# Kernel tuning notes

Measured on AMD Instinct MI355X. Metric: run time of the kernel, lower is better.

The kernel has to match this reference:

```python
import jax, jax.numpy as jnp
import numpy as np

N, S, R, M, C, CZ = 1, 128, 256, 256, 32, 128


def setup_inputs() -> dict:
    key = jax.random.key(0)
    k1, k2, k3, k4 = jax.random.split(key, 4)
    return {
        "msa_repr": jax.random.normal(k1, (N, S, R, M), dtype=jnp.float32) * 0.1,
        "left_w": jax.random.normal(k2, (M, C), dtype=jnp.float32) * 0.02,
        "right_w": jax.random.normal(k3, (M, C), dtype=jnp.float32) * 0.02,
        "out_w": jax.random.normal(k4, (C * C, CZ), dtype=jnp.float32) * 0.02,
    }


def reference(msa_repr, left_w, right_w, out_w):
    # msa_repr: [N,S,R,M]
    n, s, r, m = msa_repr.shape
    c = left_w.shape[1]
    # opm_projection: [N,S,R,M] @ [M,C] -> [N,S,R,C]
    left = jnp.einsum('nsrm,mc->nsrc', msa_repr, left_w)
    right = jnp.einsum('nsrm,mc->nsrc', msa_repr, right_w)
    # outer product summed over MSA dim s: [N,R,T,C,C]
    # (torch: a=left.transpose(-2,-3) -> [N,R,S,C]; einsum '...bac,...dae->...bdce')
    outer = jnp.einsum('nsrc,nste->nrtce', left, right).reshape(n, r, r, c * c)
    # project to pair channel: [N,R,T,C*C] @ [C*C,CZ] -> [N,R,T,CZ]
    return jnp.matmul(outer, out_w)
```

## Files before the change

### kernel.cpp

```cpp
#include <hip/hip_runtime.h>
#include <stdint.h>

#define S_DIM 128
#define R_DIM 256
#define M_DIM 256
#define C_DIM 32
#define CZ_DIM 128
#define K2_DIM 1024

typedef _Float16 f16;
typedef _Float16 f16x4 __attribute__((ext_vector_type(4)));
typedef _Float16 f16x8 __attribute__((ext_vector_type(8)));
typedef float f32x4 __attribute__((ext_vector_type(4)));
typedef float f32x16 __attribute__((ext_vector_type(16)));

typedef const __attribute__((address_space(1))) uint32_t gu32_t;
typedef __attribute__((address_space(3))) uint32_t lu32_t;
#define GLOAD_LDS16(g, l) \
    __builtin_amdgcn_global_load_lds((gu32_t*)(g), (lu32_t*)(l), 16, 0, 0)

__global__ __launch_bounds__(256, 4)
void proj_kernel(const float* __restrict__ msa, const float* __restrict__ lw,
                 const float* __restrict__ rw, const float* __restrict__ ow,
                 f16* __restrict__ left_t, f16* __restrict__ rt2,
                 f16* __restrict__ wt2) {
    __shared__ __align__(16) f16 wlT[8192];
    __shared__ __align__(16) f16 wrT[8192];

    int bid = blockIdx.x;
    int tid = threadIdx.x;
    int w = tid >> 6;
    int lane = tid & 63;
    int q = lane >> 4, li = lane & 15;
    int r  = bid >> 1;
    int s0 = (bid & 1) << 6;
    int s_col = s0 + w * 16 + li;

    const f32x4* bp = (const f32x4*)(msa + ((size_t)s_col * R_DIM + r) * M_DIM + q * 8);
    f32x4 b[16];
#pragma unroll
    for (int ks = 0; ks < 8; ks++) { b[2 * ks] = bp[ks * 8]; b[2 * ks + 1] = bp[ks * 8 + 1]; }

    {
        int i = bid * 256 + tid;
        int cz = i >> 10, k2 = i & 1023;
        int c = k2 >> 5, e = k2 & 31;
        int k2p = ((e >> 2) << 7) + (c << 2) + (e & 3);
        int ntile = cz >> 5, l31o = cz & 31;
        int kk = k2p >> 4, q5o = (k2p >> 3) & 1, j = k2p & 7;
        wt2[(ntile * 64 + kk) * 512 + (l31o * 2 + q5o) * 8 + j] = (f16)ow[k2 * CZ_DIM + cz];
    }
#pragma unroll
    for (int k = 0; k < 32; k++) {
        int i = k * 256 + tid;
        int m = i >> 5, c = i & 31;
        int d = ((m >> 3) * 32 + c) * 8 + (m & 7);
        wlT[d] = (f16)lw[i];
        wrT[d] = (f16)rw[i];
    }
    __syncthreads();

    f32x4 aL0 = {0,0,0,0}, aL1 = {0,0,0,0}, aR0 = {0,0,0,0}, aR1 = {0,0,0,0};
#pragma unroll
    for (int ks = 0; ks < 8; ks++) {
        f16x8 bf;
#pragma unroll
        for (int u = 0; u < 4; u++) { bf[u] = (f16)b[2*ks][u]; bf[4 + u] = (f16)b[2*ks+1][u]; }
        const f16* a0 = wlT + ((ks * 4 + q) * 32 + li) * 8;
        const f16* a1 = wrT + ((ks * 4 + q) * 32 + li) * 8;
        f16x8 al0 = *(const f16x8*)(a0);
        f16x8 al1 = *(const f16x8*)(a0 + 128);
        f16x8 ar0 = *(const f16x8*)(a1);
        f16x8 ar1 = *(const f16x8*)(a1 + 128);
        aL0 = __builtin_amdgcn_mfma_f32_16x16x32_f16(al0, bf, aL0, 0, 0, 0);
        aL1 = __builtin_amdgcn_mfma_f32_16x16x32_f16(al1, bf, aL1, 0, 0, 0);
        aR0 = __builtin_amdgcn_mfma_f32_16x16x32_f16(ar0, bf, aR0, 0, 0, 0);
        aR1 = __builtin_amdgcn_mfma_f32_16x16x32_f16(ar1, bf, aR1, 0, 0, 0);
    }
    int ks_s = s_col >> 4, q5_s = (s_col >> 3) & 1, j_s = s_col & 7;
    int sbase = (r * 8 + ks_s) * 512 + q5_s * 8 + j_s;
    int rl = r & 7;
    f16* Lb = left_t + (size_t)(r >> 3) * 32768;
    int sc = s_col >> 3, sj = s_col & 7;
#pragma unroll
    for (int reg = 0; reg < 4; reg++) {
        int c0 = q * 4 + reg;
        int row0 = rl * 32 + c0;
        int swz = sc ^ c0;
        Lb[(row0 * 16 + swz) * 8 + sj]        = (f16)aL0[reg];
        Lb[((row0 + 16) * 16 + swz) * 8 + sj] = (f16)aL1[reg];
        rt2[sbase + c0 * 16]        = (f16)aR0[reg];
        rt2[sbase + (c0 + 16) * 16] = (f16)aR1[reg];
    }
}

__global__ __launch_bounds__(512, 4)
void fuse_kernel(const f16* __restrict__ left_t, const f16* __restrict__ rt2,
                 const f16* __restrict__ wt2, float* __restrict__ out) {
    __shared__ __align__(16) char lds[65536];
    f16* Ls = (f16*)lds;

    int bid = blockIdx.x;
    int br = bid >> 6, bt = bid & 63;
    int tid = threadIdx.x;
    int w = tid >> 6, lane = tid & 63;
    int q5 = lane >> 5, l31 = lane & 31, lx = lane & 15;

    const f16* Lg = left_t + (size_t)br * 32768;

#pragma unroll
    for (int it = 0; it < 8; it++) {
        GLOAD_LDS16(Lg + (size_t)(it * 512 + tid) * 8, Ls + (it * 512 + tid) * 8);
    }

    int t_tile = w & 3, rg4 = w >> 2;
    int g = bt * 4 + t_tile;
    const f16* ap = rt2 + (size_t)g * 4096 + (l31 * 2 + q5) * 8;
    f16x8 afr[8];
#pragma unroll
    for (int ks = 0; ks < 8; ks++) afr[ks] = *(const f16x8*)(ap + ks * 512);

    __syncthreads();

    f32x16 acc[4] = {};
#pragma unroll
    for (int i = 0; i < 4; i++) {
        const f16* bbase = Ls + ((rg4 * 4 + i) * 32 + l31) * 128;
#pragma unroll
        for (int ks = 0; ks < 8; ks++) {
            f16x8 bfr = *(const f16x8*)(bbase + (((2 * ks + q5) ^ lx) << 3));
            acc[i] = __builtin_amdgcn_mfma_f32_32x32x16_f16(afr[ks], bfr, acc[i], 0, 0, 0);
        }
    }

    int ntile = w & 3, kh = w >> 2;
    const f16* wbase = wt2 + (size_t)(ntile * 64 + kh * 32) * 512 + (l31 * 2 + q5) * 8;
    f16x8 wfg[8][4];
#pragma unroll
    for (int u = 0; u < 4; u++) wfg[0][u] = *(const f16x8*)(wbase + u * 512);

    __syncthreads();

    int chc = l31 >> 1, bsub = 8 * (l31 & 1);
#pragma unroll
    for (int i = 0; i < 4; i++) {
        int p = (rg4 * 4 + i) * 4 + t_tile;
        char* prow = lds + p * 2048;
#pragma unroll
        for (int rg = 0; rg < 4; rg++) {
            int ch = (2 * rg + q5) * 16 + chc;
            int phys = (ch + p) & 127;
            f16x4 h = {(f16)acc[i][4 * rg], (f16)acc[i][4 * rg + 1],
                       (f16)acc[i][4 * rg + 2], (f16)acc[i][4 * rg + 3]};
            *(f16x4*)(prow + phys * 16 + bsub) = h;
        }
    }
    __syncthreads();

    const char* lbase = lds + l31 * 2048;
    int base = 64 * kh + q5 + l31;
    f16x8 afg[8][4];
    f32x16 accA = {}, accB = {};
#pragma unroll
    for (int gg = 0; gg < 8; gg++) {
        if (gg == 0) {
#pragma unroll
            for (int u = 0; u < 4; u++) wfg[1][u] = *(const f16x8*)(wbase + (4 + u) * 512);
#pragma unroll
            for (int u = 0; u < 4; u++) wfg[2][u] = *(const f16x8*)(wbase + (8 + u) * 512);
#pragma unroll
            for (int u = 0; u < 4; u++)
                afg[0][u] = *(const f16x8*)(lbase + (((base + 2 * u) & 127) << 4));
#pragma unroll
            for (int u = 0; u < 4; u++)
                afg[1][u] = *(const f16x8*)(lbase + (((base + 8 + 2 * u) & 127) << 4));
        } else {
            if (gg + 2 < 8) {
#pragma unroll
                for (int u = 0; u < 4; u++)
                    wfg[gg + 2][u] = *(const f16x8*)(wbase + ((gg + 2) * 4 + u) * 512);
            }
            if (gg + 1 < 8) {
#pragma unroll
                for (int u = 0; u < 4; u++)
                    afg[gg + 1][u] = *(const f16x8*)(lbase + (((base + (gg + 1) * 8 + 2 * u) & 127) << 4));
            }
        }
        accA = __builtin_amdgcn_mfma_f32_32x32x16_f16(afg[gg][0], wfg[gg][0], accA, 0, 0, 0);
        accB = __builtin_amdgcn_mfma_f32_32x32x16_f16(afg[gg][1], wfg[gg][1], accB, 0, 0, 0);
        accA = __builtin_amdgcn_mfma_f32_32x32x16_f16(afg[gg][2], wfg[gg][2], accA, 0, 0, 0);
        accB = __builtin_amdgcn_mfma_f32_32x32x16_f16(afg[gg][3], wfg[gg][3], accB, 0, 0, 0);
    }
    f32x16 acc2;
#pragma unroll
    for (int v = 0; v < 16; v++) acc2[v] = accA[v] + accB[v];
    __syncthreads();

    if (w >= 4) {
        char* rb = lds + (w - 4) * 4096 + lane * 64;
#pragma unroll
        for (int u = 0; u < 4; u++) {
            f32x4 part = {acc2[4 * u], acc2[4 * u + 1], acc2[4 * u + 2], acc2[4 * u + 3]};
            *(f32x4*)(rb + u * 16) = part;
        }
    }
    __syncthreads();
    if (w < 4) {
        const char* rb = lds + w * 4096 + lane * 64;
#pragma unroll
        for (int u = 0; u < 4; u++) {
            f32x4 part = *(const f32x4*)(rb + u * 16);
#pragma unroll
            for (int v = 0; v < 4; v++) acc2[4 * u + v] += part[v];
        }
        int r0 = br * 8, t0 = bt * 4, cz = w * 32 + l31;
#pragma unroll
        for (int reg = 0; reg < 16; reg++) {
            int p = (reg & 3) + 8 * (reg >> 2) + 4 * q5;
            out[((size_t)((r0 + (p >> 2)) * R_DIM + t0 + (p & 3))) * CZ_DIM + cz] = acc2[reg];
        }
    }
}

extern "C" void kernel_launch(void* const* d_in, const int* in_sizes, int n_in,
                              void* d_out, int out_size, void* d_ws, size_t ws_size,
                              hipStream_t stream) {
    const float* msa = (const float*)d_in[0];
    const float* lw  = (const float*)d_in[1];
    const float* rw  = (const float*)d_in[2];
    const float* ow  = (const float*)d_in[3];
    char* ws = (char*)d_ws;
    f16* left_t = (f16*)(ws);
    f16* rt2    = (f16*)(ws + (size_t)2 * 1024 * 1024);
    f16* wt2    = (f16*)(ws + (size_t)4 * 1024 * 1024);
    float* out  = (float*)d_out;

    proj_kernel<<<dim3(512), dim3(256), 0, stream>>>(msa, lw, rw, ow, left_t, rt2, wt2);
    fuse_kernel<<<dim3(2048), dim3(512), 0, stream>>>(left_t, rt2, wt2, out);
}
```

Baseline: 131.7 us.

## Process four row blocks per fuse workgroup with prefetched left tiles

Each fuse workgroup now loops over four consecutive row blocks. The right-side fragments and the first weight fragments are loaded once and reused across them. The next left tile is streamed into a separate LDS region while the current projection GEMM runs, using 128KB of dynamic shared memory and a launch bound of 2 waves per EU. This cuts redundant global loads and per-block setup, but it quarters the grid size and lowers occupancy, which may leave compute units underused.

```diff
diff --git a/kernel.cpp b/kernel.cpp
--- a/kernel.cpp
+++ b/kernel.cpp
@@ -94,130 +94,146 @@
     }
 }
 
-__global__ __launch_bounds__(512, 4)
+__global__ __launch_bounds__(512, 2)
 void fuse_kernel(const f16* __restrict__ left_t, const f16* __restrict__ rt2,
                  const f16* __restrict__ wt2, float* __restrict__ out) {
-    __shared__ __align__(16) char lds[65536];
+    extern __shared__ __align__(16) char lds[];
     f16* Ls = (f16*)lds;
+    char* Pr = lds + 65536;
 
     int bid = blockIdx.x;
-    int br = bid >> 6, bt = bid & 63;
+    int brq = bid >> 6, bt = bid & 63;
     int tid = threadIdx.x;
     int w = tid >> 6, lane = tid & 63;
     int q5 = lane >> 5, l31 = lane & 31, lx = lane & 15;
 
-    const f16* Lg = left_t + (size_t)br * 32768;
-
-#pragma unroll
-    for (int it = 0; it < 8; it++) {
-        GLOAD_LDS16(Lg + (size_t)(it * 512 + tid) * 8, Ls + (it * 512 + tid) * 8);
-    }
-
     int t_tile = w & 3, rg4 = w >> 2;
+    int ntile = w & 3, kh = w >> 2;
+
+    {
+        const f16* Lg = left_t + (size_t)(brq * 4) * 32768;
+#pragma unroll
+        for (int it = 0; it < 8; it++)
+            GLOAD_LDS16(Lg + (size_t)(it * 512 + tid) * 8, Ls + (it * 512 + tid) * 8);
+    }
+
     int g = bt * 4 + t_tile;
     const f16* ap = rt2 + (size_t)g * 4096 + (l31 * 2 + q5) * 8;
     f16x8 afr[8];
 #pragma unroll
     for (int ks = 0; ks < 8; ks++) afr[ks] = *(const f16x8*)(ap + ks * 512);
 
+    const f16* wbase = wt2 + (size_t)(ntile * 64 + kh * 32) * 512 + (l31 * 2 + q5) * 8;
+    const char* lbase = Pr + l31 * 2048;
+    int base = 64 * kh + q5 + l31;
+
+    f16x8 wfg[8][4];
+#pragma unroll
+    for (int u = 0; u < 4; u++) wfg[0][u] = *(const f16x8*)(wbase + u * 512);
+
     __syncthreads();
 
-    f32x16 acc[4] = {};
-#pragma unroll
-    for (int i = 0; i < 4; i++) {
-        const f16* bbase = Ls + ((rg4 * 4 + i) * 32 + l31) * 128;
-#pragma unroll
-        for (int ks = 0; ks < 8; ks++) {
-            f16x8 bfr = *(const f16x8*)(bbase + (((2 * ks + q5) ^ lx) << 3));
-            acc[i] = __builtin_amdgcn_mfma_f32_32x32x16_f16(afr[ks], bfr, acc[i], 0, 0, 0);
-        }
-    }
-
-    int ntile = w & 3, kh = w >> 2;
-    const f16* wbase = wt2 + (size_t)(ntile * 64 + kh * 32) * 512 + (l31 * 2 + q5) * 8;
-    f16x8 wfg[8][4];
-#pragma unroll
-    for (int u = 0; u < 4; u++) wfg[0][u] = *(const f16x8*)(wbase + u * 512);
-
-    __syncthreads();
-
-    int chc = l31 >> 1, bsub = 8 * (l31 & 1);
-#pragma unroll
-    for (int i = 0; i < 4; i++) {
-        int p = (rg4 * 4 + i) * 4 + t_tile;
-        char* prow = lds + p * 2048;
-#pragma unroll
-        for (int rg = 0; rg < 4; rg++) {
-            int ch = (2 * rg + q5) * 16 + chc;
-            int phys = (ch + p) & 127;
-            f16x4 h = {(f16)acc[i][4 * rg], (f16)acc[i][4 * rg + 1],
-                       (f16)acc[i][4 * rg + 2], (f16)acc[i][4 * rg + 3]};
-            *(f16x4*)(prow + phys * 16 + bsub) = h;
-        }
-    }
-    __syncthreads();
-
-    const char* lbase = lds + l31 * 2048;
-    int base = 64 * kh + q5 + l31;
-    f16x8 afg[8][4];
-    f32x16 accA = {}, accB = {};
-#pragma unroll
-    for (int gg = 0; gg < 8; gg++) {
-        if (gg == 0) {
+    for (int jr = 0; jr < 4; jr++) {
+        int br = brq * 4 + jr;
+
+        f32x16 acc[4] = {};
+#pragma unroll
+        for (int i = 0; i < 4; i++) {
+            const f16* bbase = Ls + ((rg4 * 4 + i) * 32 + l31) * 128;
+#pragma unroll
+            for (int ks = 0; ks < 8; ks++) {
+                f16x8 bfr = *(const f16x8*)(bbase + (((2 * ks + q5) ^ lx) << 3));
+                acc[i] = __builtin_amdgcn_mfma_f32_32x32x16_f16(afr[ks], bfr, acc[i], 0, 0, 0);
+            }
+        }
+
+        __syncthreads();
+
+        int chc = l31 >> 1, bsub = 8 * (l31 & 1);
+#pragma unroll
+        for (int i = 0; i < 4; i++) {
+            int p = (rg4 * 4 + i) * 4 + t_tile;
+            char* prow = Pr + p * 2048;
+#pragma unroll
+            for (int rg = 0; rg < 4; rg++) {
+                int ch = (2 * rg + q5) * 16 + chc;
+                int phys = (ch + p) & 127;
+                f16x4 h = {(f16)acc[i][4 * rg], (f16)acc[i][4 * rg + 1],
+                           (f16)acc[i][4 * rg + 2], (f16)acc[i][4 * rg + 3]};
+                *(f16x4*)(prow + phys * 16 + bsub) = h;
+            }
+        }
+        __syncthreads();
+
+        if (jr == 0) {
 #pragma unroll
             for (int u = 0; u < 4; u++) wfg[1][u] = *(const f16x8*)(wbase + (4 + u) * 512);
 #pragma unroll
             for (int u = 0; u < 4; u++) wfg[2][u] = *(const f16x8*)(wbase + (8 + u) * 512);
-#pragma unroll
-            for (int u = 0; u < 4; u++)
-                afg[0][u] = *(const f16x8*)(lbase + (((base + 2 * u) & 127) << 4));
-#pragma unroll
-            for (int u = 0; u < 4; u++)
-                afg[1][u] = *(const f16x8*)(lbase + (((base + 8 + 2 * u) & 127) << 4));
-        } else {
-            if (gg + 2 < 8) {
-#pragma unroll
-                for (int u = 0; u < 4; u++)
-                    wfg[gg + 2][u] = *(const f16x8*)(wbase + ((gg + 2) * 4 + u) * 512);
-            }
-            if (gg + 1 < 8) {
-#pragma unroll
-                for (int u = 0; u < 4; u++)
-                    afg[gg + 1][u] = *(const f16x8*)(lbase + (((base + (gg + 1) * 8 + 2 * u) & 127) << 4));
-            }
-        }
-        accA = __builtin_amdgcn_mfma_f32_32x32x16_f16(afg[gg][0], wfg[gg][0], accA, 0, 0, 0);
-        accB = __builtin_amdgcn_mfma_f32_32x32x16_f16(afg[gg][1], wfg[gg][1], accB, 0, 0, 0);
-        accA = __builtin_amdgcn_mfma_f32_32x32x16_f16(afg[gg][2], wfg[gg][2], accA, 0, 0, 0);
-        accB = __builtin_amdgcn_mfma_f32_32x32x16_f16(afg[gg][3], wfg[gg][3], accB, 0, 0, 0);
-    }
-    f32x16 acc2;
-#pragma unroll
-    for (int v = 0; v < 16; v++) acc2[v] = accA[v] + accB[v];
-    __syncthreads();
-
-    if (w >= 4) {
-        char* rb = lds + (w - 4) * 4096 + lane * 64;
-#pragma unroll
-        for (int u = 0; u < 4; u++) {
-            f32x4 part = {acc2[4 * u], acc2[4 * u + 1], acc2[4 * u + 2], acc2[4 * u + 3]};
-            *(f32x4*)(rb + u * 16) = part;
-        }
-    }
-    __syncthreads();
-    if (w < 4) {
-        const char* rb = lds + w * 4096 + lane * 64;
-#pragma unroll
-        for (int u = 0; u < 4; u++) {
-            f32x4 part = *(const f32x4*)(rb + u * 16);
-#pragma unroll
-            for (int v = 0; v < 4; v++) acc2[4 * u + v] += part[v];
-        }
-        int r0 = br * 8, t0 = bt * 4, cz = w * 32 + l31;
-#pragma unroll
-        for (int reg = 0; reg < 16; reg++) {
-            int p = (reg & 3) + 8 * (reg >> 2) + 4 * q5;
-            out[((size_t)((r0 + (p >> 2)) * R_DIM + t0 + (p & 3))) * CZ_DIM + cz] = acc2[reg];
+        }
+        f16x8 afg[8][4];
+#pragma unroll
+        for (int u = 0; u < 4; u++)
+            afg[0][u] = *(const f16x8*)(lbase + (((base + 2 * u) & 127) << 4));
+#pragma unroll
+        for (int u = 0; u < 4; u++)
+            afg[1][u] = *(const f16x8*)(lbase + (((base + 8 + 2 * u) & 127) << 4));
+
+        if (jr < 3) {
+            const f16* Lg = left_t + (size_t)(br + 1) * 32768;
+#pragma unroll
+            for (int it = 0; it < 8; it++)
+                GLOAD_LDS16(Lg + (size_t)(it * 512 + tid) * 8, Ls + (it * 512 + tid) * 8);
+        }
+
+        f32x16 accA = {}, accB = {};
+#pragma unroll
+        for (int gg = 0; gg < 8; gg++) {
+            if (gg >= 1) {
+                if (gg + 2 < 8) {
+#pragma unroll
+                    for (int u = 0; u < 4; u++)
+                        wfg[gg + 2][u] = *(const f16x8*)(wbase + ((gg + 2) * 4 + u) * 512);
+                }
+                if (gg + 1 < 8) {
+#pragma unroll
+                    for (int u = 0; u < 4; u++)
+                        afg[gg + 1][u] = *(const f16x8*)(lbase + (((base + (gg + 1) * 8 + 2 * u) & 127) << 4));
+                }
+            }
+            accA = __builtin_amdgcn_mfma_f32_32x32x16_f16(afg[gg][0], wfg[gg][0], accA, 0, 0, 0);
+            accB = __builtin_amdgcn_mfma_f32_32x32x16_f16(afg[gg][1], wfg[gg][1], accB, 0, 0, 0);
+            accA = __builtin_amdgcn_mfma_f32_32x32x16_f16(afg[gg][2], wfg[gg][2], accA, 0, 0, 0);
+            accB = __builtin_amdgcn_mfma_f32_32x32x16_f16(afg[gg][3], wfg[gg][3], accB, 0, 0, 0);
+        }
+        f32x16 acc2;
+#pragma unroll
+        for (int v = 0; v < 16; v++) acc2[v] = accA[v] + accB[v];
+        __syncthreads();
+
+        if (w >= 4) {
+            char* rb = Pr + (w - 4) * 4096 + lane * 64;
+#pragma unroll
+            for (int u = 0; u < 4; u++) {
+                f32x4 part = {acc2[4 * u], acc2[4 * u + 1], acc2[4 * u + 2], acc2[4 * u + 3]};
+                *(f32x4*)(rb + u * 16) = part;
+            }
+        }
+        __syncthreads();
+        if (w < 4) {
+            const char* rb = Pr + w * 4096 + lane * 64;
+#pragma unroll
+            for (int u = 0; u < 4; u++) {
+                f32x4 part = *(const f32x4*)(rb + u * 16);
+#pragma unroll
+                for (int v = 0; v < 4; v++) acc2[4 * u + v] += part[v];
+            }
+            int r0 = br * 8, t0 = bt * 4, cz = w * 32 + l31;
+#pragma unroll
+            for (int reg = 0; reg < 16; reg++) {
+                int p = (reg & 3) + 8 * (reg >> 2) + 4 * q5;
+                out[((size_t)((r0 + (p >> 2)) * R_DIM + t0 + (p & 3))) * CZ_DIM + cz] = acc2[reg];
+            }
         }
     }
 }
@@ -235,6 +251,13 @@
     f16* wt2    = (f16*)(ws + (size_t)4 * 1024 * 1024);
     float* out  = (float*)d_out;
 
+    static bool attr_set = false;
+    if (!attr_set) {
+        hipFuncSetAttribute((const void*)fuse_kernel,
+                            hipFuncAttributeMaxDynamicSharedMemorySize, 131072);
+        attr_set = true;
+    }
+
     proj_kernel<<<dim3(512), dim3(256), 0, stream>>>(msa, lw, rw, ow, left_t, rt2, wt2);
-    fuse_kernel<<<dim3(2048), dim3(512), 0, stream>>>(left_t, rt2, wt2, out);
+    fuse_kernel<<<dim3(512), dim3(512), 131072, stream>>>(left_t, rt2, wt2, out);
 }
```

Result: slower. 164.1 us (+24.6%).
